# Kernel tuning notes

Hardware: AMD Instinct MI355X
Metric: run time of the kernel (lower is better)

## Reference

```python
import jax, jax.numpy as jnp
import numpy as np

N_NODES = 50000


def _gcn_conv(x, src, dst, W, b, num_nodes):
    """PyG GCNConv: out = D^{-1/2}(A+I)D^{-1/2} (x @ W) + b, self-loops added."""
    h = x @ W  # [N, out]
    # degrees over edges incl. self-loops (src/dst already include self-loops)
    ones = jnp.ones(src.shape[0], dtype=h.dtype)
    deg = jax.ops.segment_sum(ones, dst, num_segments=num_nodes)
    dinv = jnp.where(deg > 0, jax.lax.rsqrt(deg), 0.0)
    norm = dinv[src] * dinv[dst]  # [E]
    msgs = h[src] * norm[:, None]  # [E, out] gather (memory-bound)
    out = jax.ops.segment_sum(msgs, dst, num_segments=num_nodes)
    return out + b


def setup_inputs() -> dict:
    key = jax.random.key(0)
    ks = jax.random.split(key, 8)
    in_c, h2, h1, out_c = 256, 256, 128, 128
    x = jax.random.normal(ks[0], (N_NODES, in_c), dtype=jnp.float32)
    edge_index = jax.random.randint(ks[1], (2, 800000), 0, N_NODES, dtype=jnp.int64)
    def glorot(k, fi, fo):
        s = float(np.sqrt(6.0 / (fi + fo)))
        return jax.random.uniform(k, (fi, fo), jnp.float32, -s, s)
    return {
        "x": x,
        "edge_index": edge_index,
        "W1": glorot(ks[2], in_c, h2), "b1": jnp.zeros((h2,), jnp.float32),
        "W2": glorot(ks[3], h2, h1), "b2": jnp.zeros((h1,), jnp.float32),
        "W3": glorot(ks[4], h1, out_c), "b3": jnp.zeros((out_c,), jnp.float32),
    }


def reference(x, edge_index, W1, b1, W2, b2, W3, b3):
    n = x.shape[0]
    loops = jnp.arange(n, dtype=edge_index.dtype)
    src = jnp.concatenate([edge_index[0], loops])
    dst = jnp.concatenate([edge_index[1], loops])
    # dropout is a no-op in eval mode (training=False)
    h1 = jax.nn.relu(_gcn_conv(x, src, dst, W1, b1, n))
    h2 = jax.nn.relu(_gcn_conv(h1, src, dst, W2, b2, n))
    h3 = jax.nn.relu(_gcn_conv(h2, src, dst, W3, b3, n))
    return jnp.concatenate([h1, h2, h3], axis=1)
```

## Files before the change

### kernel.cpp

```cpp
#include <hip/hip_runtime.h>

typedef __attribute__((ext_vector_type(8))) short bfrag8;
typedef __attribute__((ext_vector_type(4))) float f32x4v;
typedef __attribute__((ext_vector_type(4))) int   i32x4v;

__device__ inline short f2bf(float f) {
    unsigned u = __builtin_bit_cast(unsigned, f);
    u = (u + 0x7FFFu + ((u >> 16) & 1u)) >> 16;
    return (short)u;
}
__device__ inline float bf2f(short s) {
    unsigned u = ((unsigned)(unsigned short)s) << 16;
    return __builtin_bit_cast(float, u);
}
__device__ inline int pack2(short lo, short hi) {
    return (int)(((unsigned)(unsigned short)lo) | (((unsigned)(unsigned short)hi) << 16));
}
__device__ inline int pad16i(int v) { return (v + 15) & ~15; }


__global__ void block_sum_kernel(const int* __restrict__ deg, int n, int* __restrict__ bsums) {
    int i = blockIdx.x * 256 + threadIdx.x;
    int v = (i < n) ? pad16i(deg[i] + 1) : 0;
#pragma unroll
    for (int off = 32; off > 0; off >>= 1) v += __shfl_down(v, off);
    __shared__ int wsum[4];
    int lane = threadIdx.x & 63, w = threadIdx.x >> 6;
    if (lane == 0) wsum[w] = v;
    __syncthreads();
    if (threadIdx.x == 0) bsums[blockIdx.x] = wsum[0] + wsum[1] + wsum[2] + wsum[3];
}

__global__ void scan_final_kernel(const int* __restrict__ deg, int n, int B,
                                  const int* __restrict__ bsums,
                                  int* __restrict__ offs, int* __restrict__ cursor,
                                  float* __restrict__ dinv, int* __restrict__ csr) {
    __shared__ int sb[256];
    __shared__ int s[256];
    int tid = threadIdx.x;
    sb[tid] = (tid < B) ? bsums[tid] : 0;
    __syncthreads();
    for (int off = 1; off < 256; off <<= 1) {
        int t = (tid >= off) ? sb[tid - off] : 0;
        __syncthreads();
        sb[tid] += t;
        __syncthreads();
    }
    int myBase = (blockIdx.x == 0) ? 0 : sb[blockIdx.x - 1];
    int total = sb[255];
    int i = blockIdx.x * 256 + tid;
    int vt = (i < n) ? deg[i] + 1 : 0;
    int pv = (i < n) ? pad16i(vt) : 0;
    s[tid] = pv;
    __syncthreads();
    for (int off = 1; off < 256; off <<= 1) {
        int t = (tid >= off) ? s[tid - off] : 0;
        __syncthreads();
        s[tid] += t;
        __syncthreads();
    }
    if (i < n) {
        int excl = s[tid] - pv + myBase;
        offs[i] = excl;
        csr[excl] = i;
        cursor[i] = excl + 1;
        for (int p = excl + vt; p < excl + pv; ++p) csr[p] = n;
        dinv[i] = rsqrtf((float)vt);
    } else if (i < gridDim.x * 256) {
        dinv[i] = 0.f;
    }
    if (blockIdx.x == 0 && tid == 0) offs[n] = total;
}


__global__ void prep_kernel(const int* __restrict__ dst, int E, int* __restrict__ deg,
                            const float* __restrict__ x, short* __restrict__ xb,
                            int total8, int totalp8,
                            const float* __restrict__ W1, short* __restrict__ Wt1,
                            const float* __restrict__ W2, short* __restrict__ Wt2,
                            const float* __restrict__ W3, short* __restrict__ Wt3) {
    int g = blockIdx.x * blockDim.x + threadIdx.x;
    if (g < E) {
        atomicAdd(&deg[dst[g]], 1);
        return;
    }
    int i = g - E;
    if (i < total8) {
        const float4* p = (const float4*)(x + (size_t)i * 8);
        float4 v0 = p[0], v1 = p[1];
        int4 w = make_int4(pack2(f2bf(v0.x), f2bf(v0.y)), pack2(f2bf(v0.z), f2bf(v0.w)),
                           pack2(f2bf(v1.x), f2bf(v1.y)), pack2(f2bf(v1.z), f2bf(v1.w)));
        *(int4*)(xb + (size_t)i * 8) = w;
    } else if (i < totalp8) {
        *(int4*)(xb + (size_t)i * 8) = make_int4(0, 0, 0, 0);
    } else {
        int j = i - totalp8;
        if (j < 65536) {
            int k = j >> 8, c = j & 255;
            Wt1[c * 256 + k] = f2bf(W1[j]);
        } else if (j < 65536 + 32768) {
            int m = j - 65536;
            int k = m >> 7, c = m & 127;
            Wt2[c * 256 + k] = f2bf(W2[m]);
        } else if (j < 65536 + 32768 + 16384) {
            int m = j - 65536 - 32768;
            int k = m >> 7, c = m & 127;
            Wt3[c * 128 + k] = f2bf(W3[m]);
        }
    }
}


template<int K>
__device__ __forceinline__ void gemm_body(
        const short* __restrict__ A, const short* __restrict__ Bt,
        const float* __restrict__ dinv, short* __restrict__ Tout, int ldt,
        int bx, int by, char* bsb) {
    const int tid = threadIdx.x;
    const int lane = tid & 63;
    const int wid = tid >> 6;
    const int l15 = lane & 15;
    const int quad = lane >> 4;
    const int q8 = quad * 8;
    const int bn = by * 128;
    const int row0 = bx * 256 + wid * 64;

    {
        constexpr int TOT16 = 128 * K / 8;
#pragma unroll
        for (int i = tid; i < TOT16; i += 256) {
            int r = i / (K / 8);
            int c = (i % (K / 8)) * 8;
            int byteoff = (r * K + c) * 2;
            byteoff ^= (r & 7) << 4;
            *(int4*)(bsb + byteoff) = *(const int4*)&Bt[(size_t)(bn + r) * K + c];
        }
    }
    __syncthreads();

    f32x4v acc[4][8];
#pragma unroll
    for (int i = 0; i < 4; ++i)
#pragma unroll
        for (int j = 0; j < 8; ++j) acc[i][j] = (f32x4v){0.f, 0.f, 0.f, 0.f};

    const short* aBase = A + (size_t)(row0 + l15) * K + q8;

#pragma unroll
    for (int ks = 0; ks < K / 32; ++ks) {
        bfrag8 af[4], bf[8];
#pragma unroll
        for (int mt = 0; mt < 4; ++mt)
            af[mt] = *(const bfrag8*)(aBase + (size_t)mt * 16 * K + ks * 32);
#pragma unroll
        for (int nt = 0; nt < 8; ++nt) {
            int r = nt * 16 + l15;
            int byteoff = (r * K + ks * 32 + q8) * 2;
            byteoff ^= (r & 7) << 4;
            bf[nt] = *(const bfrag8*)(bsb + byteoff);
        }
#pragma unroll
        for (int mt = 0; mt < 4; ++mt)
#pragma unroll
            for (int nt = 0; nt < 8; ++nt)
                acc[mt][nt] = __builtin_amdgcn_mfma_f32_16x16x32_bf16(af[mt], bf[nt], acc[mt][nt], 0, 0, 0);
    }

#pragma unroll
    for (int mt = 0; mt < 4; ++mt) {
#pragma unroll
        for (int r = 0; r < 4; ++r) {
            int grow = row0 + mt * 16 + quad * 4 + r;
            float di = dinv[grow];
            short* outp = Tout + (size_t)grow * ldt + bn + l15;
#pragma unroll
            for (int nt = 0; nt < 8; ++nt)
                outp[nt * 16] = f2bf(acc[mt][nt][r] * di);
        }
    }
}

template<int K>
__global__ __launch_bounds__(256, 2) void gemm_skinny_kernel(
        const short* __restrict__ A, const short* __restrict__ Bt,
        const float* __restrict__ dinv, short* __restrict__ Tout, int ldt) {
    __shared__ short Bs[128 * K];
    gemm_body<K>(A, Bt, dinv, Tout, ldt, blockIdx.x, blockIdx.y, (char*)Bs);
}

template<int K>
__global__ __launch_bounds__(256, 2) void gemm_csr_kernel(
        const short* __restrict__ A, const short* __restrict__ Bt,
        const float* __restrict__ dinv, short* __restrict__ Tout, int ldt, int tilesX,
        const int* __restrict__ src, const int* __restrict__ dst, int E,
        int* __restrict__ cursor, int* __restrict__ csr, int csrBlocks) {
    __shared__ short Bs[128 * K];
    if ((int)blockIdx.x < csrBlocks) {
        int e = blockIdx.x * 256 + threadIdx.x;
        if (e < E) {
            int d = dst[e];
            int p = atomicAdd(&cursor[d], 1);
            csr[p] = src[e];
        }
        return;
    }
    int tile = blockIdx.x - csrBlocks;
    gemm_body<K>(A, Bt, dinv, Tout, ldt, tile % tilesX, tile / tilesX, (char*)Bs);
}


template<bool WB>
__global__ __launch_bounds__(256) void agg256_kernel(
        const short* __restrict__ hn, const float* __restrict__ dinv,
        const int* __restrict__ offs, const int* __restrict__ csr,
        const float* __restrict__ bias, float* __restrict__ out,
        short* __restrict__ hb, int coloff, int n) {
    int node = blockIdx.x * 4 + (threadIdx.x >> 6);
    if (node >= n) return;
    int lane = threadIdx.x & 63;
    int hl = lane & 31;
    int sub = lane >> 5;
    const short* base = hn + hl * 8;

    float acc[8];
#pragma unroll
    for (int v = 0; v < 8; ++v) acc[v] = 0.f;

    int beg = offs[node], end = offs[node + 1];
    for (int e = beg + sub; e < end; e += 16) {
        int s[8];
#pragma unroll
        for (int j = 0; j < 8; ++j) s[j] = __builtin_nontemporal_load(csr + e + 2 * j);
        bfrag8 r[8];
#pragma unroll
        for (int j = 0; j < 8; ++j) r[j] = *(const bfrag8*)(base + (size_t)s[j] * 256);
#pragma unroll
        for (int j = 0; j < 8; ++j)
#pragma unroll
            for (int v = 0; v < 8; ++v) acc[v] += bf2f(r[j][v]);
    }

#pragma unroll
    for (int v = 0; v < 8; ++v) acc[v] += __shfl_xor(acc[v], 32);

    if (sub == 0) {
        float di = dinv[node];
        float res[8];
#pragma unroll
        for (int v = 0; v < 8; ++v)
            res[v] = fmaxf(fmaf(di, acc[v], bias[hl * 8 + v]), 0.f);
        float* op = out + (size_t)node * 512 + coloff + hl * 8;
        f32x4v w0 = {res[0], res[1], res[2], res[3]};
        f32x4v w1 = {res[4], res[5], res[6], res[7]};
        __builtin_nontemporal_store(w0, (f32x4v*)op);
        __builtin_nontemporal_store(w1, (f32x4v*)(op + 4));
        if (WB) {
            i32x4v w = {pack2(f2bf(res[0]), f2bf(res[1])), pack2(f2bf(res[2]), f2bf(res[3])),
                        pack2(f2bf(res[4]), f2bf(res[5])), pack2(f2bf(res[6]), f2bf(res[7]))};
            __builtin_nontemporal_store(w, (i32x4v*)(hb + (size_t)node * 256 + hl * 8));
        }
    }
}


template<bool WB>
__global__ __launch_bounds__(256) void agg128_kernel(
        const short* __restrict__ hn, const float* __restrict__ dinv,
        const int* __restrict__ offs, const int* __restrict__ csr,
        const float* __restrict__ bias, float* __restrict__ out,
        short* __restrict__ hb, int coloff, int n, int npad) {
    int node = blockIdx.x * 4 + (threadIdx.x >> 6);
    int lane = threadIdx.x & 63;
    if (node >= n) {
        if (WB && node < npad) ((int*)(hb + (size_t)node * 128))[lane] = 0;
        return;
    }
    int ch = lane & 15;
    int sub = lane >> 4;
    const short* base = hn + ch * 8;

    float acc[8];
#pragma unroll
    for (int v = 0; v < 8; ++v) acc[v] = 0.f;

    int beg = offs[node], end = offs[node + 1];
    int e = beg + sub;
    for (; e + 16 < end; e += 32) {
        int s[8];
#pragma unroll
        for (int j = 0; j < 8; ++j) s[j] = __builtin_nontemporal_load(csr + e + 4 * j);
        bfrag8 r[8];
#pragma unroll
        for (int j = 0; j < 8; ++j) r[j] = *(const bfrag8*)(base + (size_t)s[j] * 128);
#pragma unroll
        for (int j = 0; j < 8; ++j)
#pragma unroll
            for (int v = 0; v < 8; ++v) acc[v] += bf2f(r[j][v]);
    }
    if (e < end) {
        int s[4];
#pragma unroll
        for (int j = 0; j < 4; ++j) s[j] = __builtin_nontemporal_load(csr + e + 4 * j);
        bfrag8 r[4];
#pragma unroll
        for (int j = 0; j < 4; ++j) r[j] = *(const bfrag8*)(base + (size_t)s[j] * 128);
#pragma unroll
        for (int j = 0; j < 4; ++j)
#pragma unroll
            for (int v = 0; v < 8; ++v) acc[v] += bf2f(r[j][v]);
    }

#pragma unroll
    for (int v = 0; v < 8; ++v) {
        acc[v] += __shfl_xor(acc[v], 16);
        acc[v] += __shfl_xor(acc[v], 32);
    }

    if (sub == 0) {
        float di = dinv[node];
        float res[8];
#pragma unroll
        for (int v = 0; v < 8; ++v)
            res[v] = fmaxf(fmaf(di, acc[v], bias[ch * 8 + v]), 0.f);
        float* op = out + (size_t)node * 512 + coloff + ch * 8;
        f32x4v w0 = {res[0], res[1], res[2], res[3]};
        f32x4v w1 = {res[4], res[5], res[6], res[7]};
        __builtin_nontemporal_store(w0, (f32x4v*)op);
        __builtin_nontemporal_store(w1, (f32x4v*)(op + 4));
        if (WB) {
            i32x4v w = {pack2(f2bf(res[0]), f2bf(res[1])), pack2(f2bf(res[2]), f2bf(res[3])),
                        pack2(f2bf(res[4]), f2bf(res[5])), pack2(f2bf(res[6]), f2bf(res[7]))};
            __builtin_nontemporal_store(w, (i32x4v*)(hb + (size_t)node * 128 + ch * 8));
        }
    }
}


extern "C" void kernel_launch(void* const* d_in, const int* in_sizes, int n_in,
                              void* d_out, int out_size, void* d_ws, size_t ws_size,
                              hipStream_t stream) {
    const float* x  = (const float*)d_in[0];
    const int*   ei = (const int*)d_in[1];
    const float* W1 = (const float*)d_in[2];
    const float* b1 = (const float*)d_in[3];
    const float* W2 = (const float*)d_in[4];
    const float* b2 = (const float*)d_in[5];
    const float* W3 = (const float*)d_in[6];
    const float* b3 = (const float*)d_in[7];

    const int IN_C = 256, H2 = 256, H1 = 128, OUT_C = 128;
    int n = in_sizes[0] / IN_C;
    int E = in_sizes[1] / 2;
    const int* src = ei;
    const int* dst = ei + E;

    int sb = (n + 255) / 256;
    int npad = sb * 256;

    char* ws = (char*)d_ws;
    auto carve = [&](size_t bytes) { char* p = ws; ws += (bytes + 255) & ~(size_t)255; return p; };
    int*   deg    = (int*)  carve((size_t)n * 4);
    int*   offs   = (int*)  carve(((size_t)n + 1) * 4);
    int*   cursor = (int*)  carve((size_t)n * 4);
    float* dinv   = (float*)carve((size_t)npad * 4);
    int*   csr    = (int*)  carve(((size_t)E + 16 * (size_t)n) * 4);
    int*   bsums  = (int*)  carve(256 * 4);
    short* Wt1    = (short*)carve((size_t)IN_C * H2 * 2);
    short* Wt2    = (short*)carve((size_t)H2 * H1 * 2);
    short* Wt3    = (short*)carve((size_t)H1 * OUT_C * 2);
    short* t      = (short*)carve((size_t)npad * 256 * 2);
    short* inb    = (short*)carve((size_t)npad * 256 * 2);

    float* out = (float*)d_out;
    int nblk = (n + 255) / 256;

    hipMemsetAsync(deg, 0, (size_t)n * sizeof(int), stream);

    int total8 = n * IN_C / 8;
    int totalp8 = npad * IN_C / 8;
    int prepTot = E + totalp8 + 65536 + 32768 + 16384;
    prep_kernel<<<(prepTot + 255) / 256, 256, 0, stream>>>(
        dst, E, deg, x, inb, total8, totalp8, W1, Wt1, W2, Wt2, W3, Wt3);

    block_sum_kernel<<<nblk, 256, 0, stream>>>(deg, n, bsums);
    scan_final_kernel<<<nblk, 256, 0, stream>>>(deg, n, nblk, bsums, offs, cursor, dinv, csr);

    int csrBlocks = (E + 255) / 256;
    int gemmTiles = sb * (H2 / 128);
    gemm_csr_kernel<256><<<csrBlocks + gemmTiles, 256, 0, stream>>>(
        inb, Wt1, dinv, t, H2, sb, src, dst, E, cursor, csr, csrBlocks);
    agg256_kernel<true><<<(n + 3) / 4, 256, 0, stream>>>(t, dinv, offs, csr, b1, out, inb, 0, n);

    gemm_skinny_kernel<256><<<dim3(sb, H1 / 128), 256, 0, stream>>>(inb, Wt2, dinv, t, H1);
    agg128_kernel<true><<<(npad + 3) / 4, 256, 0, stream>>>(t, dinv, offs, csr, b2, out, inb, H2, n, npad);

    gemm_skinny_kernel<128><<<dim3(sb, OUT_C / 128), 256, 0, stream>>>(inb, Wt3, dinv, t, OUT_C);
    agg128_kernel<false><<<(n + 3) / 4, 256, 0, stream>>>(t, dinv, offs, csr, b3, out, nullptr, H2 + H1, n, npad);
}
```

Measured before the change: 403.6 us.

## Fuse layer aggregation with next-layer GEMM through shared-memory tiles

Each aggregation kernel now handles a 64-node tile. It writes the ReLU'd bf16 activations into swizzled LDS instead of global memory, then runs the next layer's MFMA GEMM directly from LDS and writes the dinv-scaled transformed features. This drops two standalone GEMM launches and the global round-trip of the intermediate bf16 activations. In exchange, each block handles 64 nodes serially per wave (16 per wave), so gather parallelism and occupancy drop, and the weight fragments are read from global memory without LDS staging.

```diff
diff --git a/kernel.cpp b/kernel.cpp
--- a/kernel.cpp
+++ b/kernel.cpp
@@ -181,14 +181,6 @@
 }
 
 template<int K>
-__global__ __launch_bounds__(256, 2) void gemm_skinny_kernel(
-        const short* __restrict__ A, const short* __restrict__ Bt,
-        const float* __restrict__ dinv, short* __restrict__ Tout, int ldt) {
-    __shared__ short Bs[128 * K];
-    gemm_body<K>(A, Bt, dinv, Tout, ldt, blockIdx.x, blockIdx.y, (char*)Bs);
-}
-
-template<int K>
 __global__ __launch_bounds__(256, 2) void gemm_csr_kernel(
         const short* __restrict__ A, const short* __restrict__ Bt,
         const float* __restrict__ dinv, short* __restrict__ Tout, int ldt, int tilesX,
@@ -209,72 +201,238 @@
 }
 
 
-template<bool WB>
-__global__ __launch_bounds__(256) void agg256_kernel(
-        const short* __restrict__ hn, const float* __restrict__ dinv,
+__global__ __launch_bounds__(256) void aggmm256_kernel(
+        const short* __restrict__ t1, const float* __restrict__ dinv,
         const int* __restrict__ offs, const int* __restrict__ csr,
-        const float* __restrict__ bias, float* __restrict__ out,
-        short* __restrict__ hb, int coloff, int n) {
-    int node = blockIdx.x * 4 + (threadIdx.x >> 6);
-    if (node >= n) return;
-    int lane = threadIdx.x & 63;
-    int hl = lane & 31;
-    int sub = lane >> 5;
-    const short* base = hn + hl * 8;
-
-    float acc[8];
-#pragma unroll
-    for (int v = 0; v < 8; ++v) acc[v] = 0.f;
-
-    int beg = offs[node], end = offs[node + 1];
-    for (int e = beg + sub; e < end; e += 16) {
-        int s[8];
-#pragma unroll
-        for (int j = 0; j < 8; ++j) s[j] = __builtin_nontemporal_load(csr + e + 2 * j);
-        bfrag8 r[8];
-#pragma unroll
-        for (int j = 0; j < 8; ++j) r[j] = *(const bfrag8*)(base + (size_t)s[j] * 256);
-#pragma unroll
-        for (int j = 0; j < 8; ++j)
-#pragma unroll
-            for (int v = 0; v < 8; ++v) acc[v] += bf2f(r[j][v]);
-    }
-
-#pragma unroll
-    for (int v = 0; v < 8; ++v) acc[v] += __shfl_xor(acc[v], 32);
-
-    if (sub == 0) {
-        float di = dinv[node];
-        float res[8];
-#pragma unroll
-        for (int v = 0; v < 8; ++v)
-            res[v] = fmaxf(fmaf(di, acc[v], bias[hl * 8 + v]), 0.f);
-        float* op = out + (size_t)node * 512 + coloff + hl * 8;
-        f32x4v w0 = {res[0], res[1], res[2], res[3]};
-        f32x4v w1 = {res[4], res[5], res[6], res[7]};
-        __builtin_nontemporal_store(w0, (f32x4v*)op);
-        __builtin_nontemporal_store(w1, (f32x4v*)(op + 4));
-        if (WB) {
-            i32x4v w = {pack2(f2bf(res[0]), f2bf(res[1])), pack2(f2bf(res[2]), f2bf(res[3])),
-                        pack2(f2bf(res[4]), f2bf(res[5])), pack2(f2bf(res[6]), f2bf(res[7]))};
-            __builtin_nontemporal_store(w, (i32x4v*)(hb + (size_t)node * 256 + hl * 8));
-        }
-    }
-}
-
-
-template<bool WB>
+        const float* __restrict__ bias, const short* __restrict__ Wt2,
+        float* __restrict__ out, short* __restrict__ t2, int n) {
+    __shared__ short h1s[64 * 256];
+    char* hsb = (char*)h1s;
+    const int tid = threadIdx.x;
+    const int lane = tid & 63;
+    const int wid = tid >> 6;
+    const int hl = lane & 31;
+    const int sub = lane >> 5;
+    const int base = blockIdx.x * 64;
+    const short* gb = t1 + hl * 8;
+
+    for (int i = 0; i < 16; ++i) {
+        int row = wid * 16 + i;
+        int node = base + row;
+        int lbyte = (row * 512 + hl * 16) ^ ((row & 7) << 4);
+        if (node < n) {
+            float acc[8];
+#pragma unroll
+            for (int v = 0; v < 8; ++v) acc[v] = 0.f;
+            int beg = offs[node], end = offs[node + 1];
+            for (int e = beg + sub; e < end; e += 16) {
+                int s[8];
+#pragma unroll
+                for (int j = 0; j < 8; ++j) s[j] = __builtin_nontemporal_load(csr + e + 2 * j);
+                bfrag8 r[8];
+#pragma unroll
+                for (int j = 0; j < 8; ++j) r[j] = *(const bfrag8*)(gb + (size_t)s[j] * 256);
+#pragma unroll
+                for (int j = 0; j < 8; ++j)
+#pragma unroll
+                    for (int v = 0; v < 8; ++v) acc[v] += bf2f(r[j][v]);
+            }
+#pragma unroll
+            for (int v = 0; v < 8; ++v) acc[v] += __shfl_xor(acc[v], 32);
+            if (sub == 0) {
+                float di = dinv[node];
+                float res[8];
+#pragma unroll
+                for (int v = 0; v < 8; ++v)
+                    res[v] = fmaxf(fmaf(di, acc[v], bias[hl * 8 + v]), 0.f);
+                float* op = out + (size_t)node * 512 + hl * 8;
+                f32x4v w0 = {res[0], res[1], res[2], res[3]};
+                f32x4v w1 = {res[4], res[5], res[6], res[7]};
+                __builtin_nontemporal_store(w0, (f32x4v*)op);
+                __builtin_nontemporal_store(w1, (f32x4v*)(op + 4));
+                i32x4v w = {pack2(f2bf(res[0]), f2bf(res[1])), pack2(f2bf(res[2]), f2bf(res[3])),
+                            pack2(f2bf(res[4]), f2bf(res[5])), pack2(f2bf(res[6]), f2bf(res[7]))};
+                *(i32x4v*)(hsb + lbyte) = w;
+            }
+        } else if (sub == 0) {
+            i32x4v z = {0, 0, 0, 0};
+            *(i32x4v*)(hsb + lbyte) = z;
+        }
+    }
+    __syncthreads();
+
+    const int l15 = lane & 15;
+    const int quad = lane >> 4;
+    const int q8 = quad * 8;
+    const int wn0 = wid * 32;
+    f32x4v acc2[4][2];
+#pragma unroll
+    for (int i = 0; i < 4; ++i)
+#pragma unroll
+        for (int j = 0; j < 2; ++j) acc2[i][j] = (f32x4v){0.f, 0.f, 0.f, 0.f};
+#pragma unroll
+    for (int ks = 0; ks < 8; ++ks) {
+        bfrag8 af[4], bf[2];
+#pragma unroll
+        for (int mt = 0; mt < 4; ++mt) {
+            int row = mt * 16 + l15;
+            int byteoff = (row * 512 + ks * 64 + q8 * 2) ^ ((row & 7) << 4);
+            af[mt] = *(const bfrag8*)(hsb + byteoff);
+        }
+#pragma unroll
+        for (int nt = 0; nt < 2; ++nt) {
+            int col = wn0 + nt * 16 + l15;
+            bf[nt] = *(const bfrag8*)(Wt2 + (size_t)col * 256 + ks * 32 + q8);
+        }
+#pragma unroll
+        for (int mt = 0; mt < 4; ++mt)
+#pragma unroll
+            for (int nt = 0; nt < 2; ++nt)
+                acc2[mt][nt] = __builtin_amdgcn_mfma_f32_16x16x32_bf16(af[mt], bf[nt], acc2[mt][nt], 0, 0, 0);
+    }
+#pragma unroll
+    for (int mt = 0; mt < 4; ++mt) {
+#pragma unroll
+        for (int r = 0; r < 4; ++r) {
+            int grow = base + mt * 16 + quad * 4 + r;
+            float di = dinv[grow];
+            short* tp = t2 + (size_t)grow * 128 + wn0 + l15;
+#pragma unroll
+            for (int nt = 0; nt < 2; ++nt)
+                tp[nt * 16] = f2bf(acc2[mt][nt][r] * di);
+        }
+    }
+}
+
+
+__global__ __launch_bounds__(256) void aggmm128_kernel(
+        const short* __restrict__ t2, const float* __restrict__ dinv,
+        const int* __restrict__ offs, const int* __restrict__ csr,
+        const float* __restrict__ bias, const short* __restrict__ Wt3,
+        float* __restrict__ out, short* __restrict__ t3, int n) {
+    __shared__ short h2s[64 * 128];
+    char* hsb = (char*)h2s;
+    const int tid = threadIdx.x;
+    const int lane = tid & 63;
+    const int wid = tid >> 6;
+    const int ch = lane & 15;
+    const int sub = lane >> 4;
+    const int base = blockIdx.x * 64;
+    const short* gb = t2 + ch * 8;
+
+    for (int i = 0; i < 16; ++i) {
+        int row = wid * 16 + i;
+        int node = base + row;
+        int lbyte = (row * 256 + ch * 16) ^ ((row & 7) << 4);
+        if (node < n) {
+            float acc[8];
+#pragma unroll
+            for (int v = 0; v < 8; ++v) acc[v] = 0.f;
+            int beg = offs[node], end = offs[node + 1];
+            int e = beg + sub;
+            for (; e + 16 < end; e += 32) {
+                int s[8];
+#pragma unroll
+                for (int j = 0; j < 8; ++j) s[j] = __builtin_nontemporal_load(csr + e + 4 * j);
+                bfrag8 r[8];
+#pragma unroll
+                for (int j = 0; j < 8; ++j) r[j] = *(const bfrag8*)(gb + (size_t)s[j] * 128);
+#pragma unroll
+                for (int j = 0; j < 8; ++j)
+#pragma unroll
+                    for (int v = 0; v < 8; ++v) acc[v] += bf2f(r[j][v]);
+            }
+            if (e < end) {
+                int s[4];
+#pragma unroll
+                for (int j = 0; j < 4; ++j) s[j] = __builtin_nontemporal_load(csr + e + 4 * j);
+                bfrag8 r[4];
+#pragma unroll
+                for (int j = 0; j < 4; ++j) r[j] = *(const bfrag8*)(gb + (size_t)s[j] * 128);
+#pragma unroll
+                for (int j = 0; j < 4; ++j)
+#pragma unroll
+                    for (int v = 0; v < 8; ++v) acc[v] += bf2f(r[j][v]);
+            }
+#pragma unroll
+            for (int v = 0; v < 8; ++v) {
+                acc[v] += __shfl_xor(acc[v], 16);
+                acc[v] += __shfl_xor(acc[v], 32);
+            }
+            if (sub == 0) {
+                float di = dinv[node];
+                float res[8];
+#pragma unroll
+                for (int v = 0; v < 8; ++v)
+                    res[v] = fmaxf(fmaf(di, acc[v], bias[ch * 8 + v]), 0.f);
+                float* op = out + (size_t)node * 512 + 256 + ch * 8;
+                f32x4v w0 = {res[0], res[1], res[2], res[3]};
+                f32x4v w1 = {res[4], res[5], res[6], res[7]};
+                __builtin_nontemporal_store(w0, (f32x4v*)op);
+                __builtin_nontemporal_store(w1, (f32x4v*)(op + 4));
+                i32x4v w = {pack2(f2bf(res[0]), f2bf(res[1])), pack2(f2bf(res[2]), f2bf(res[3])),
+                            pack2(f2bf(res[4]), f2bf(res[5])), pack2(f2bf(res[6]), f2bf(res[7]))};
+                *(i32x4v*)(hsb + lbyte) = w;
+            }
+        } else if (sub == 0) {
+            i32x4v z = {0, 0, 0, 0};
+            *(i32x4v*)(hsb + lbyte) = z;
+        }
+    }
+    __syncthreads();
+
+    const int l15 = lane & 15;
+    const int quad = lane >> 4;
+    const int q8 = quad * 8;
+    const int wn0 = wid * 32;
+    f32x4v acc2[4][2];
+#pragma unroll
+    for (int i = 0; i < 4; ++i)
+#pragma unroll
+        for (int j = 0; j < 2; ++j) acc2[i][j] = (f32x4v){0.f, 0.f, 0.f, 0.f};
+#pragma unroll
+    for (int ks = 0; ks < 4; ++ks) {
+        bfrag8 af[4], bf[2];
+#pragma unroll
+        for (int mt = 0; mt < 4; ++mt) {
+            int row = mt * 16 + l15;
+            int byteoff = (row * 256 + ks * 64 + q8 * 2) ^ ((row & 7) << 4);
+            af[mt] = *(const bfrag8*)(hsb + byteoff);
+        }
+#pragma unroll
+        for (int nt = 0; nt < 2; ++nt) {
+            int col = wn0 + nt * 16 + l15;
+            bf[nt] = *(const bfrag8*)(Wt3 + (size_t)col * 128 + ks * 32 + q8);
+        }
+#pragma unroll
+        for (int mt = 0; mt < 4; ++mt)
+#pragma unroll
+            for (int nt = 0; nt < 2; ++nt)
+                acc2[mt][nt] = __builtin_amdgcn_mfma_f32_16x16x32_bf16(af[mt], bf[nt], acc2[mt][nt], 0, 0, 0);
+    }
+#pragma unroll
+    for (int mt = 0; mt < 4; ++mt) {
+#pragma unroll
+        for (int r = 0; r < 4; ++r) {
+            int grow = base + mt * 16 + quad * 4 + r;
+            float di = dinv[grow];
+            short* tp = t3 + (size_t)grow * 128 + wn0 + l15;
+#pragma unroll
+            for (int nt = 0; nt < 2; ++nt)
+                tp[nt * 16] = f2bf(acc2[mt][nt][r] * di);
+        }
+    }
+}
+
+
 __global__ __launch_bounds__(256) void agg128_kernel(
         const short* __restrict__ hn, const float* __restrict__ dinv,
         const int* __restrict__ offs, const int* __restrict__ csr,
         const float* __restrict__ bias, float* __restrict__ out,
-        short* __restrict__ hb, int coloff, int n, int npad) {
+        int coloff, int n) {
     int node = blockIdx.x * 4 + (threadIdx.x >> 6);
+    if (node >= n) return;
     int lane = threadIdx.x & 63;
-    if (node >= n) {
-        if (WB && node < npad) ((int*)(hb + (size_t)node * 128))[lane] = 0;
-        return;
-    }
     int ch = lane & 15;
     int sub = lane >> 4;
     const short* base = hn + ch * 8;
@@ -327,11 +485,6 @@
         f32x4v w1 = {res[4], res[5], res[6], res[7]};
         __builtin_nontemporal_store(w0, (f32x4v*)op);
         __builtin_nontemporal_store(w1, (f32x4v*)(op + 4));
-        if (WB) {
-            i32x4v w = {pack2(f2bf(res[0]), f2bf(res[1])), pack2(f2bf(res[2]), f2bf(res[3])),
-                        pack2(f2bf(res[4]), f2bf(res[5])), pack2(f2bf(res[6]), f2bf(res[7]))};
-            __builtin_nontemporal_store(w, (i32x4v*)(hb + (size_t)node * 128 + ch * 8));
-        }
     }
 }
 
@@ -368,8 +521,10 @@
     short* Wt1    = (short*)carve((size_t)IN_C * H2 * 2);
     short* Wt2    = (short*)carve((size_t)H2 * H1 * 2);
     short* Wt3    = (short*)carve((size_t)H1 * OUT_C * 2);
-    short* t      = (short*)carve((size_t)npad * 256 * 2);
-    short* inb    = (short*)carve((size_t)npad * 256 * 2);
+    short* t1     = (short*)carve((size_t)npad * 256 * 2);
+    short* t2     = (short*)carve((size_t)npad * 128 * 2);
+    short* t3     = (short*)carve((size_t)npad * 128 * 2);
+    short* xb     = (short*)carve((size_t)npad * 256 * 2);
 
     float* out = (float*)d_out;
     int nblk = (n + 255) / 256;
@@ -380,7 +535,7 @@
     int totalp8 = npad * IN_C / 8;
     int prepTot = E + totalp8 + 65536 + 32768 + 16384;
     prep_kernel<<<(prepTot + 255) / 256, 256, 0, stream>>>(
-        dst, E, deg, x, inb, total8, totalp8, W1, Wt1, W2, Wt2, W3, Wt3);
+        dst, E, deg, x, xb, total8, totalp8, W1, Wt1, W2, Wt2, W3, Wt3);
 
     block_sum_kernel<<<nblk, 256, 0, stream>>>(deg, n, bsums);
     scan_final_kernel<<<nblk, 256, 0, stream>>>(deg, n, nblk, bsums, offs, cursor, dinv, csr);
@@ -388,12 +543,12 @@
     int csrBlocks = (E + 255) / 256;
     int gemmTiles = sb * (H2 / 128);
     gemm_csr_kernel<256><<<csrBlocks + gemmTiles, 256, 0, stream>>>(
-        inb, Wt1, dinv, t, H2, sb, src, dst, E, cursor, csr, csrBlocks);
-    agg256_kernel<true><<<(n + 3) / 4, 256, 0, stream>>>(t, dinv, offs, csr, b1, out, inb, 0, n);
-
-    gemm_skinny_kernel<256><<<dim3(sb, H1 / 128), 256, 0, stream>>>(inb, Wt2, dinv, t, H1);
-    agg128_kernel<true><<<(npad + 3) / 4, 256, 0, stream>>>(t, dinv, offs, csr, b2, out, inb, H2, n, npad);
-
-    gemm_skinny_kernel<128><<<dim3(sb, OUT_C / 128), 256, 0, stream>>>(inb, Wt3, dinv, t, OUT_C);
-    agg128_kernel<false><<<(n + 3) / 4, 256, 0, stream>>>(t, dinv, offs, csr, b3, out, nullptr, H2 + H1, n, npad);
-}
+        xb, Wt1, dinv, t1, H2, sb, src, dst, E, cursor, csr, csrBlocks);
+
+    int nb64 = (n + 63) / 64;
+    aggmm256_kernel<<<nb64, 256, 0, stream>>>(t1, dinv, offs, csr, b1, Wt2, out, t2, n);
+
+    aggmm128_kernel<<<nb64, 256, 0, stream>>>(t2, dinv, offs, csr, b2, Wt3, out, t3, n);
+
+    agg128_kernel<<<(n + 3) / 4, 256, 0, stream>>>(t3, dinv, offs, csr, b3, out, H2 + H1, n);
+}
```

Result: slower. 445.3 us (+10.4%).

## Narrow first-layer GEMM tiles to 64 columns and raise occupancy

Applied to the files above, without the earlier changes.

The fused CSR-fill plus first GEMM kernel now uses 256x64 output tiles with a padded (non-swizzled) shared-memory B tile, halving accumulators per thread and allowing launch bounds of 4 blocks per SM. This doubles the number of GEMM tiles to improve latency hiding and load balance alongside the CSR atomic scatter blocks. A separate bf16 input buffer is also added so the layer-1 input no longer aliases the buffer the aggregation writes into. The cost is that A rows are re-read twice as often across the column tiles, and the extra buffer uses more workspace.

```diff
diff --git a/kernel.cpp b/kernel.cpp
--- a/kernel.cpp
+++ b/kernel.cpp
@@ -112,18 +112,20 @@
 
 
 template<int K>
-__device__ __forceinline__ void gemm_body(
+__global__ __launch_bounds__(256, 2) void gemm_skinny_kernel(
         const short* __restrict__ A, const short* __restrict__ Bt,
-        const float* __restrict__ dinv, short* __restrict__ Tout, int ldt,
-        int bx, int by, char* bsb) {
+        const float* __restrict__ dinv, short* __restrict__ Tout, int ldt) {
+    __shared__ short Bs[128 * K];
+    char* bsb = (char*)Bs;
+
     const int tid = threadIdx.x;
     const int lane = tid & 63;
     const int wid = tid >> 6;
     const int l15 = lane & 15;
     const int quad = lane >> 4;
     const int q8 = quad * 8;
-    const int bn = by * 128;
-    const int row0 = bx * 256 + wid * 64;
+    const int bn = blockIdx.y * 128;
+    const int row0 = blockIdx.x * 256 + wid * 64;
 
     {
         constexpr int TOT16 = 128 * K / 8;
@@ -180,21 +182,15 @@
     }
 }
 
+
 template<int K>
-__global__ __launch_bounds__(256, 2) void gemm_skinny_kernel(
-        const short* __restrict__ A, const short* __restrict__ Bt,
-        const float* __restrict__ dinv, short* __restrict__ Tout, int ldt) {
-    __shared__ short Bs[128 * K];
-    gemm_body<K>(A, Bt, dinv, Tout, ldt, blockIdx.x, blockIdx.y, (char*)Bs);
-}
-
-template<int K>
-__global__ __launch_bounds__(256, 2) void gemm_csr_kernel(
+__global__ __launch_bounds__(256, 4) void gemm_csr_kernel(
         const short* __restrict__ A, const short* __restrict__ Bt,
         const float* __restrict__ dinv, short* __restrict__ Tout, int ldt, int tilesX,
         const int* __restrict__ src, const int* __restrict__ dst, int E,
         int* __restrict__ cursor, int* __restrict__ csr, int csrBlocks) {
-    __shared__ short Bs[128 * K];
+    constexpr int BSTR = K + 8;
+    __shared__ short Bs[64 * BSTR];
     if ((int)blockIdx.x < csrBlocks) {
         int e = blockIdx.x * 256 + threadIdx.x;
         if (e < E) {
@@ -205,7 +201,64 @@
         return;
     }
     int tile = blockIdx.x - csrBlocks;
-    gemm_body<K>(A, Bt, dinv, Tout, ldt, tile % tilesX, tile / tilesX, (char*)Bs);
+    const int bx = tile % tilesX, by = tile / tilesX;
+
+    const int tid = threadIdx.x;
+    const int lane = tid & 63;
+    const int wid = tid >> 6;
+    const int l15 = lane & 15;
+    const int quad = lane >> 4;
+    const int q8 = quad * 8;
+    const int bn = by * 64;
+    const int row0 = bx * 256 + wid * 64;
+
+    {
+        constexpr int TOT16 = 64 * K / 8;
+#pragma unroll
+        for (int i = tid; i < TOT16; i += 256) {
+            int r = i / (K / 8);
+            int c = (i % (K / 8)) * 8;
+            *(int4*)&Bs[r * BSTR + c] = *(const int4*)&Bt[(size_t)(bn + r) * K + c];
+        }
+    }
+    __syncthreads();
+
+    f32x4v acc[4][4];
+#pragma unroll
+    for (int i = 0; i < 4; ++i)
+#pragma unroll
+        for (int j = 0; j < 4; ++j) acc[i][j] = (f32x4v){0.f, 0.f, 0.f, 0.f};
+
+    const short* aBase = A + (size_t)(row0 + l15) * K + q8;
+
+#pragma unroll
+    for (int ks = 0; ks < K / 32; ++ks) {
+        bfrag8 af[4], bf[4];
+#pragma unroll
+        for (int mt = 0; mt < 4; ++mt)
+            af[mt] = *(const bfrag8*)(aBase + (size_t)mt * 16 * K + ks * 32);
+#pragma unroll
+        for (int nt = 0; nt < 4; ++nt)
+            bf[nt] = *(const bfrag8*)&Bs[(nt * 16 + l15) * BSTR + ks * 32 + q8];
+#pragma unroll
+        for (int mt = 0; mt < 4; ++mt)
+#pragma unroll
+            for (int nt = 0; nt < 4; ++nt)
+                acc[mt][nt] = __builtin_amdgcn_mfma_f32_16x16x32_bf16(af[mt], bf[nt], acc[mt][nt], 0, 0, 0);
+    }
+
+#pragma unroll
+    for (int mt = 0; mt < 4; ++mt) {
+#pragma unroll
+        for (int r = 0; r < 4; ++r) {
+            int grow = row0 + mt * 16 + quad * 4 + r;
+            float di = dinv[grow];
+            short* outp = Tout + (size_t)grow * ldt + bn + l15;
+#pragma unroll
+            for (int nt = 0; nt < 4; ++nt)
+                outp[nt * 16] = f2bf(acc[mt][nt][r] * di);
+        }
+    }
 }
 
 
@@ -368,6 +421,7 @@
     short* Wt1    = (short*)carve((size_t)IN_C * H2 * 2);
     short* Wt2    = (short*)carve((size_t)H2 * H1 * 2);
     short* Wt3    = (short*)carve((size_t)H1 * OUT_C * 2);
+    short* xb     = (short*)carve((size_t)npad * 256 * 2);
     short* t      = (short*)carve((size_t)npad * 256 * 2);
     short* inb    = (short*)carve((size_t)npad * 256 * 2);
 
@@ -380,15 +434,16 @@
     int totalp8 = npad * IN_C / 8;
     int prepTot = E + totalp8 + 65536 + 32768 + 16384;
     prep_kernel<<<(prepTot + 255) / 256, 256, 0, stream>>>(
-        dst, E, deg, x, inb, total8, totalp8, W1, Wt1, W2, Wt2, W3, Wt3);
+        dst, E, deg, x, xb, total8, totalp8, W1, Wt1, W2, Wt2, W3, Wt3);
 
     block_sum_kernel<<<nblk, 256, 0, stream>>>(deg, n, bsums);
     scan_final_kernel<<<nblk, 256, 0, stream>>>(deg, n, nblk, bsums, offs, cursor, dinv, csr);
 
     int csrBlocks = (E + 255) / 256;
-    int gemmTiles = sb * (H2 / 128);
+    int gemmTiles = sb * (H2 / 64);
     gemm_csr_kernel<256><<<csrBlocks + gemmTiles, 256, 0, stream>>>(
-        inb, Wt1, dinv, t, H2, sb, src, dst, E, cursor, csr, csrBlocks);
+        xb, Wt1, dinv, t, H2, sb, src, dst, E, cursor, csr, csrBlocks);
+
     agg256_kernel<true><<<(n + 3) / 4, 256, 0, stream>>>(t, dinv, offs, csr, b1, out, inb, 0, n);
 
     gemm_skinny_kernel<256><<<dim3(sb, H1 / 128), 256, 0, stream>>>(inb, Wt2, dinv, t, H1);
```

Result: slower. 415.6 us (+3.0%).

## Partition degree and CSR-fill atomics into eight node ranges per block group

Applied to the files above, without the earlier changes.

The degree-count and CSR-fill atomics now run in eight groups of blocks, interleaved by block index. Each group scans every edge and only performs the atomic when the destination falls in its own eighth of the node range. The aim is to concentrate atomic traffic on a smaller address window at any one time, improving cache locality and spreading the atomics across XCD caches. In exchange, each edge's dst is read eight times instead of once. The bf16 copy of x also gets its own buffer, separate from the one the later layers reuse.

```diff
diff --git a/kernel.cpp b/kernel.cpp
--- a/kernel.cpp
+++ b/kernel.cpp
@@ -74,17 +74,28 @@
 
 
 __global__ void prep_kernel(const int* __restrict__ dst, int E, int* __restrict__ deg,
+                            int degBlocks, int range,
                             const float* __restrict__ x, short* __restrict__ xb,
                             int total8, int totalp8,
                             const float* __restrict__ W1, short* __restrict__ Wt1,
                             const float* __restrict__ W2, short* __restrict__ Wt2,
                             const float* __restrict__ W3, short* __restrict__ Wt3) {
-    int g = blockIdx.x * blockDim.x + threadIdx.x;
-    if (g < E) {
-        atomicAdd(&deg[dst[g]], 1);
+    if ((int)blockIdx.x < degBlocks) {
+        int g = blockIdx.x & 7;
+        int gthreads = (degBlocks >> 3) * 256;
+        int base = (blockIdx.x >> 3) * 256 + threadIdx.x;
+        int lo = g * range;
+#pragma unroll
+        for (int it = 0; it < 8; ++it) {
+            int e = base + it * gthreads;
+            if (e < E) {
+                int d = dst[e];
+                if ((unsigned)(d - lo) < (unsigned)range) atomicAdd(&deg[d], 1);
+            }
+        }
         return;
     }
-    int i = g - E;
+    int i = (blockIdx.x - degBlocks) * 256 + threadIdx.x;
     if (i < total8) {
         const float4* p = (const float4*)(x + (size_t)i * 8);
         float4 v0 = p[0], v1 = p[1];
@@ -193,14 +204,23 @@
         const short* __restrict__ A, const short* __restrict__ Bt,
         const float* __restrict__ dinv, short* __restrict__ Tout, int ldt, int tilesX,
         const int* __restrict__ src, const int* __restrict__ dst, int E,
-        int* __restrict__ cursor, int* __restrict__ csr, int csrBlocks) {
+        int* __restrict__ cursor, int* __restrict__ csr, int csrBlocks, int range) {
     __shared__ short Bs[128 * K];
     if ((int)blockIdx.x < csrBlocks) {
-        int e = blockIdx.x * 256 + threadIdx.x;
-        if (e < E) {
-            int d = dst[e];
-            int p = atomicAdd(&cursor[d], 1);
-            csr[p] = src[e];
+        int g = blockIdx.x & 7;
+        int gthreads = (csrBlocks >> 3) * 256;
+        int base = (blockIdx.x >> 3) * 256 + threadIdx.x;
+        int lo = g * range;
+#pragma unroll
+        for (int it = 0; it < 8; ++it) {
+            int e = base + it * gthreads;
+            if (e < E) {
+                int d = dst[e];
+                if ((unsigned)(d - lo) < (unsigned)range) {
+                    int p = atomicAdd(&cursor[d], 1);
+                    csr[p] = src[e];
+                }
+            }
         }
         return;
     }
@@ -368,6 +388,7 @@
     short* Wt1    = (short*)carve((size_t)IN_C * H2 * 2);
     short* Wt2    = (short*)carve((size_t)H2 * H1 * 2);
     short* Wt3    = (short*)carve((size_t)H1 * OUT_C * 2);
+    short* xb     = (short*)carve((size_t)npad * 256 * 2);
     short* t      = (short*)carve((size_t)npad * 256 * 2);
     short* inb    = (short*)carve((size_t)npad * 256 * 2);
 
@@ -376,19 +397,29 @@
 
     hipMemsetAsync(deg, 0, (size_t)n * sizeof(int), stream);
 
+    int range8 = (n + 7) / 8;
+    int bpg = (E + 8 * 256 - 1) / (8 * 256);
+    if (bpg < 1) bpg = 1;
+    bpg = (bpg + 0);
+    int degBlocks = ((bpg + 0) * 8);
+    while (8 * (degBlocks >> 3) * 256 < E) degBlocks += 8;
+
     int total8 = n * IN_C / 8;
     int totalp8 = npad * IN_C / 8;
-    int prepTot = E + totalp8 + 65536 + 32768 + 16384;
-    prep_kernel<<<(prepTot + 255) / 256, 256, 0, stream>>>(
-        dst, E, deg, x, inb, total8, totalp8, W1, Wt1, W2, Wt2, W3, Wt3);
+    int restTot = totalp8 + 65536 + 32768 + 16384;
+    int prepBlocks = degBlocks + (restTot + 255) / 256;
+    prep_kernel<<<prepBlocks, 256, 0, stream>>>(
+        dst, E, deg, degBlocks, range8, x, xb, total8, totalp8,
+        W1, Wt1, W2, Wt2, W3, Wt3);
 
     block_sum_kernel<<<nblk, 256, 0, stream>>>(deg, n, bsums);
     scan_final_kernel<<<nblk, 256, 0, stream>>>(deg, n, nblk, bsums, offs, cursor, dinv, csr);
 
-    int csrBlocks = (E + 255) / 256;
+    int csrBlocks = degBlocks;
     int gemmTiles = sb * (H2 / 128);
     gemm_csr_kernel<256><<<csrBlocks + gemmTiles, 256, 0, stream>>>(
-        inb, Wt1, dinv, t, H2, sb, src, dst, E, cursor, csr, csrBlocks);
+        xb, Wt1, dinv, t, H2, sb, src, dst, E, cursor, csr, csrBlocks, range8);
+
     agg256_kernel<true><<<(n + 3) / 4, 256, 0, stream>>>(t, dinv, offs, csr, b1, out, inb, 0, n);
 
     gemm_skinny_kernel<256><<<dim3(sb, H1 / 128), 256, 0, stream>>>(inb, Wt2, dinv, t, H1);
```

Result: no change. 407.2 us (+0.9%).
